# Performance work log

Hardware: AMD Instinct MI355X
Metric: run time of the kernel (lower is better)

## Reference

```python
import jax, jax.numpy as jnp
import numpy as np

N_NODES = 50000
N_EDGES = 800000
IN_CH = 256
OUT_CH = 64  # heads=1
NEG_SLOPE = 0.2


def setup_inputs() -> dict:
    key = jax.random.key(0)
    k1, k2, k3, k4, k5 = jax.random.split(key, 5)
    x = jax.random.normal(k1, (N_NODES, IN_CH), dtype=jnp.float32)
    edge_index = jax.random.randint(k2, (2, N_EDGES), 0, N_NODES, dtype=jnp.int64)
    # glorot init for dense weight [out, in] (torch Linear layout) and att [out, 2]
    s_w = np.sqrt(6.0 / (OUT_CH + IN_CH)).astype(np.float32)
    W = jax.random.uniform(k3, (OUT_CH, IN_CH), minval=-s_w, maxval=s_w, dtype=jnp.float32)
    b = jnp.zeros((OUT_CH,), dtype=jnp.float32)
    s_a = np.sqrt(6.0 / (OUT_CH + 2)).astype(np.float32)
    att = jax.random.uniform(k4, (OUT_CH, 2), minval=-s_a, maxval=s_a, dtype=jnp.float32)
    return {"x": x, "edge_index": edge_index, "W": W, "b": b, "att": att}


def reference(x, edge_index, W, b, att):
    n = x.shape[0]
    # dense projection: feature [N, OUT_CH]
    feature = x @ W.T + b
    # per-node attention contributions: e_pre [N, 2]
    e_pre = feature @ att
    tar = edge_index[0]  # flow='target_to_source'
    src = edge_index[1]
    # edge logit = leakyrelu(a_tar(t) + a_src(s)); self-loop logit per node
    logit_edge = jax.nn.leaky_relu(e_pre[tar, 0] + e_pre[src, 1], NEG_SLOPE)
    logit_self = jax.nn.leaky_relu(e_pre[:, 0] + e_pre[:, 1], NEG_SLOPE)
    # segment softmax over {self edge} U {incoming edges} per target node
    m = jnp.maximum(jax.ops.segment_max(logit_edge, tar, num_segments=n), logit_self)
    exp_edge = jnp.exp(logit_edge - m[tar])
    exp_self = jnp.exp(logit_self - m)
    denom = exp_self + jax.ops.segment_sum(exp_edge, tar, num_segments=n)
    alpha = exp_edge / denom[tar]          # [E]
    alpha_self = exp_self / denom          # [N]
    # weighted gather-scatter aggregation (fused_gas_agg)
    msgs = alpha[:, None] * feature[src]   # [E, OUT_CH]
    out = alpha_self[:, None] * feature + jax.ops.segment_sum(msgs, tar, num_segments=n)
    return out
```

## Files before the change

### kernel.cpp

```cpp
#include <hip/hip_runtime.h>
#include <math.h>

#define N_NODES 50000
#define N_EDGES 800000
#define IN_CH 256
#define OUT_CH 64
#define NEG_SLOPE 0.2f
#define PAD 64
#define DEGS 16

#define EDGE_BLOCKS 196
#define GEMM_BLOCKS 782

typedef __bf16 bf16x4 __attribute__((ext_vector_type(4)));
typedef __bf16 bf16x8 __attribute__((ext_vector_type(8)));
typedef float  f32x4  __attribute__((ext_vector_type(4)));

__global__ __launch_bounds__(256) void k_zero(int* __restrict__ deg)
{
    int idx = (blockIdx.x * 256 + threadIdx.x) * 4;
    if (idx + 4 <= N_NODES * DEGS)
        *reinterpret_cast<int4*>(&deg[idx]) = make_int4(0, 0, 0, 0);
}

__global__ __launch_bounds__(256) void k_fused(
    const float* __restrict__ x, const float* __restrict__ W,
    const float* __restrict__ bias, const float* __restrict__ att,
    const int* __restrict__ ei,
    __bf16* __restrict__ featb, float* __restrict__ e0,
    float* __restrict__ e1, int* __restrict__ deg,
    unsigned short* __restrict__ pcsr)
{
    __shared__ __bf16 B[64][264];

    const int t = threadIdx.x;

    if (blockIdx.x < EDGE_BLOCKS) {
        const int base = blockIdx.x * 4096 + t * 4;
        int tn[16], sn[16], sl[16];
        #pragma unroll
        for (int c = 0; c < 4; ++c) {
            int e = base + c * 1024;
            if (e + 4 <= N_EDGES) {
                *reinterpret_cast<int4*>(&tn[c * 4]) =
                    *reinterpret_cast<const int4*>(&ei[e]);
                *reinterpret_cast<int4*>(&sn[c * 4]) =
                    *reinterpret_cast<const int4*>(&ei[N_EDGES + e]);
            } else {
                #pragma unroll
                for (int j = 0; j < 4; ++j) {
                    int ee = e + j;
                    tn[c * 4 + j] = (ee < N_EDGES) ? ei[ee] : -1;
                    sn[c * 4 + j] = (ee < N_EDGES) ? ei[N_EDGES + ee] : 0;
                }
            }
        }
        #pragma unroll
        for (int k = 0; k < 16; ++k)
            sl[k] = (tn[k] >= 0) ? atomicAdd(&deg[tn[k] * DEGS], 1) : 0x7fffffff;
        #pragma unroll
        for (int k = 0; k < 16; ++k)
            if (tn[k] >= 0 && sl[k] < PAD)
                pcsr[(size_t)tn[k] * PAD + sl[k]] = (unsigned short)sn[k];
        return;
    }

    const int row0 = (blockIdx.x - EDGE_BLOCKS) * 64;
    const int wv   = t >> 6;
    const int li   = t & 63;
    const int lm   = li & 15;
    const int lq   = li >> 4;

    {
        const int sr = t >> 2;
        const int cq = t & 3;
        #pragma unroll
        for (int j = 0; j < 4; ++j) {
            #pragma unroll
            for (int i = 0; i < 4; ++i) {
                int kk = j * 64 + cq * 16 + i * 4;
                float4 w1 = *reinterpret_cast<const float4*>(&W[(size_t)sr * IN_CH + kk]);
                bf16x4 g = {(__bf16)w1.x, (__bf16)w1.y, (__bf16)w1.z, (__bf16)w1.w};
                *reinterpret_cast<bf16x4*>(&B[sr][kk]) = g;
            }
        }
    }
    __syncthreads();

    const int myrow = row0 + wv * 16 + lm;
    const float* xrow = x + (size_t)(myrow < N_NODES ? myrow : 0) * IN_CH;

    f32x4 acc[4];
    #pragma unroll
    for (int tn = 0; tn < 4; ++tn) acc[tn] = (f32x4){0.f, 0.f, 0.f, 0.f};

    #pragma unroll
    for (int kb = 0; kb < 8; ++kb) {
        int ko = kb * 32 + lq * 8;
        float4 a0 = *reinterpret_cast<const float4*>(&xrow[ko]);
        float4 a1 = *reinterpret_cast<const float4*>(&xrow[ko + 4]);
        bf16x8 a = {(__bf16)a0.x, (__bf16)a0.y, (__bf16)a0.z, (__bf16)a0.w,
                    (__bf16)a1.x, (__bf16)a1.y, (__bf16)a1.z, (__bf16)a1.w};
        #pragma unroll
        for (int tn = 0; tn < 4; ++tn) {
            bf16x8 b = *reinterpret_cast<const bf16x8*>(&B[tn * 16 + lm][ko]);
            acc[tn] = __builtin_amdgcn_mfma_f32_16x16x32_bf16(a, b, acc[tn], 0, 0, 0);
        }
    }

    float att0[4], att1[4], bv[4];
    #pragma unroll
    for (int tn = 0; tn < 4; ++tn) {
        int c = tn * 16 + lm;
        att0[tn] = att[c * 2 + 0];
        att1[tn] = att[c * 2 + 1];
        bv[tn]   = bias[c];
    }

    float p0[4] = {0.f, 0.f, 0.f, 0.f};
    float p1[4] = {0.f, 0.f, 0.f, 0.f};
    #pragma unroll
    for (int r = 0; r < 4; ++r) {
        int row = row0 + wv * 16 + lq * 4 + r;
        #pragma unroll
        for (int tn = 0; tn < 4; ++tn) {
            float f = acc[tn][r] + bv[tn];
            if (row < N_NODES)
                featb[(size_t)row * OUT_CH + tn * 16 + lm] = (__bf16)f;
            p0[r] += f * att0[tn];
            p1[r] += f * att1[tn];
        }
    }

    #pragma unroll
    for (int m = 1; m < 16; m <<= 1) {
        #pragma unroll
        for (int r = 0; r < 4; ++r) {
            p0[r] += __shfl_xor(p0[r], m, 64);
            p1[r] += __shfl_xor(p1[r], m, 64);
        }
    }
    if (lm == 0) {
        #pragma unroll
        for (int r = 0; r < 4; ++r) {
            int row = row0 + wv * 16 + lq * 4 + r;
            if (row < N_NODES) {
                e0[row] = p0[r];
                e1[row] = p1[r];
            }
        }
    }
}

__global__ __launch_bounds__(256) void k_gather(
    const float* __restrict__ e0, const float* __restrict__ e1,
    const __bf16* __restrict__ featb, const int* __restrict__ deg,
    const unsigned short* __restrict__ pcsr, float* __restrict__ out)
{
    int t    = blockIdx.x * 4 + (threadIdx.x >> 6);
    int lane = threadIdx.x & 63;
    if (t >= N_NODES) return;

    const int g  = lane >> 4;
    const int cl = lane & 15;

    int cnt = deg[t * DEGS];
    cnt = cnt > PAD ? PAD : cnt;

    float e0t = e0[t];

    int si = (int)pcsr[(size_t)t * PAD + lane];
    si = (lane < cnt) ? si : 0;
    float qi = e1[si];
    float zi = e0t + qi;
    float wi = (lane < cnt) ? __expf(zi > 0.f ? zi : NEG_SLOPE * zi) : 0.f;

    float zs  = e0t + e1[t];
    float wsf = __expf(zs > 0.f ? zs : NEG_SLOPE * zs);
    bf16x4 sf = *reinterpret_cast<const bf16x4*>(&featb[(size_t)t * OUT_CH + cl * 4]);

    float wsum = wi;
    #pragma unroll
    for (int m = 1; m < 64; m <<= 1)
        wsum += __shfl_xor(wsum, m, 64);
    wsum += wsf;

    f32x4 acc = {0.f, 0.f, 0.f, 0.f};
    int i = 0;
    for (; i + 16 <= cnt; i += 16) {
        float a0 = 0.f, a1 = 0.f, a2 = 0.f, a3 = 0.f;
        int   s0 = __shfl(si, i + g,      64);
        int   s1 = __shfl(si, i + 4 + g,  64);
        int   s2 = __shfl(si, i + 8 + g,  64);
        int   s3 = __shfl(si, i + 12 + g, 64);
        float w0 = __shfl(wi, i + g,      64);
        float w1 = __shfl(wi, i + 4 + g,  64);
        float w2 = __shfl(wi, i + 8 + g,  64);
        float w3 = __shfl(wi, i + 12 + g, 64);
        bf16x4 f0 = *reinterpret_cast<const bf16x4*>(&featb[(size_t)s0 * OUT_CH + cl * 4]);
        bf16x4 f1 = *reinterpret_cast<const bf16x4*>(&featb[(size_t)s1 * OUT_CH + cl * 4]);
        bf16x4 f2 = *reinterpret_cast<const bf16x4*>(&featb[(size_t)s2 * OUT_CH + cl * 4]);
        bf16x4 f3 = *reinterpret_cast<const bf16x4*>(&featb[(size_t)s3 * OUT_CH + cl * 4]);
        #pragma unroll
        for (int j = 0; j < 4; ++j) {
            a0 += 0.f;
            acc[j] += w0 * (float)f0[j] + w1 * (float)f1[j]
                    + w2 * (float)f2[j] + w3 * (float)f3[j];
        }
        (void)a0; (void)a1; (void)a2; (void)a3;
    }
    #pragma unroll 2
    for (; i < cnt; i += 4) {
        int   s0 = __shfl(si, i + g, 64);
        float w0 = __shfl(wi, i + g, 64);
        bf16x4 f0 = *reinterpret_cast<const bf16x4*>(&featb[(size_t)s0 * OUT_CH + cl * 4]);
        #pragma unroll
        for (int j = 0; j < 4; ++j)
            acc[j] += w0 * (float)f0[j];
    }

    #pragma unroll
    for (int j = 0; j < 4; ++j) {
        acc[j] += __shfl_xor(acc[j], 16, 64);
        acc[j] += __shfl_xor(acc[j], 32, 64);
    }

    if (g == 0) {
        float inv = 1.f / wsum;
        float4 o;
        o.x = (acc[0] + wsf * (float)sf[0]) * inv;
        o.y = (acc[1] + wsf * (float)sf[1]) * inv;
        o.z = (acc[2] + wsf * (float)sf[2]) * inv;
        o.w = (acc[3] + wsf * (float)sf[3]) * inv;
        *reinterpret_cast<float4*>(&out[(size_t)t * OUT_CH + cl * 4]) = o;
    }
}

extern "C" void kernel_launch(void* const* d_in, const int* in_sizes, int n_in,
                              void* d_out, int out_size, void* d_ws, size_t ws_size,
                              hipStream_t stream)
{
    const float* x    = (const float*)d_in[0];
    const int*   ei   = (const int*)d_in[1];
    const float* W    = (const float*)d_in[2];
    const float* bias = (const float*)d_in[3];
    const float* att  = (const float*)d_in[4];
    float* out = (float*)d_out;

    __bf16* featb = (__bf16*)d_ws;
    float*  e0    = (float*)(featb + (size_t)N_NODES * OUT_CH);
    float*  e1    = e0 + N_NODES;
    int*    deg   = (int*)(e1 + N_NODES);
    unsigned short* pcsr = (unsigned short*)(deg + (size_t)N_NODES * DEGS);

    dim3 blk(256);

    k_zero<<<dim3((N_NODES * DEGS / 4 + 255) / 256), blk, 0, stream>>>(deg);

    k_fused<<<dim3(EDGE_BLOCKS + GEMM_BLOCKS), blk, 0, stream>>>(
        x, W, bias, att, ei, featb, e0, e1, deg, pcsr);

    k_gather<<<dim3((N_NODES + 3) / 4), blk, 0, stream>>>(
        e0, e1, featb, deg, pcsr, out);
}
```

Baseline: 162.6 us.

## Stage e1 as fp16 in LDS and make gather a persistent grid-stride kernel

Result: slower. 175.3 us (+7.8%).

```diff
diff --git a/kernel.cpp b/kernel.cpp
--- a/kernel.cpp
+++ b/kernel.cpp
@@ -12,9 +12,13 @@
 #define EDGE_BLOCKS 196
 #define GEMM_BLOCKS 782
 
+#define GATHER_BLOCKS 256
+#define GATHER_THREADS 1024
+
 typedef __bf16 bf16x4 __attribute__((ext_vector_type(4)));
 typedef __bf16 bf16x8 __attribute__((ext_vector_type(8)));
 typedef float  f32x4  __attribute__((ext_vector_type(4)));
+typedef _Float16 f16x4 __attribute__((ext_vector_type(4)));
 
 __global__ __launch_bounds__(256) void k_zero(int* __restrict__ deg)
 {
@@ -152,87 +156,96 @@
     }
 }
 
-__global__ __launch_bounds__(256) void k_gather(
+__global__ __launch_bounds__(GATHER_THREADS) void k_gather(
     const float* __restrict__ e0, const float* __restrict__ e1,
     const __bf16* __restrict__ featb, const int* __restrict__ deg,
     const unsigned short* __restrict__ pcsr, float* __restrict__ out)
 {
-    int t    = blockIdx.x * 4 + (threadIdx.x >> 6);
-    int lane = threadIdx.x & 63;
-    if (t >= N_NODES) return;
-
-    const int g  = lane >> 4;
-    const int cl = lane & 15;
-
-    int cnt = deg[t * DEGS];
-    cnt = cnt > PAD ? PAD : cnt;
-
-    float e0t = e0[t];
-
-    int si = (int)pcsr[(size_t)t * PAD + lane];
-    si = (lane < cnt) ? si : 0;
-    float qi = e1[si];
-    float zi = e0t + qi;
-    float wi = (lane < cnt) ? __expf(zi > 0.f ? zi : NEG_SLOPE * zi) : 0.f;
-
-    float zs  = e0t + e1[t];
-    float wsf = __expf(zs > 0.f ? zs : NEG_SLOPE * zs);
-    bf16x4 sf = *reinterpret_cast<const bf16x4*>(&featb[(size_t)t * OUT_CH + cl * 4]);
-
-    float wsum = wi;
-    #pragma unroll
-    for (int m = 1; m < 64; m <<= 1)
-        wsum += __shfl_xor(wsum, m, 64);
-    wsum += wsf;
-
-    f32x4 acc = {0.f, 0.f, 0.f, 0.f};
-    int i = 0;
-    for (; i + 16 <= cnt; i += 16) {
-        float a0 = 0.f, a1 = 0.f, a2 = 0.f, a3 = 0.f;
-        int   s0 = __shfl(si, i + g,      64);
-        int   s1 = __shfl(si, i + 4 + g,  64);
-        int   s2 = __shfl(si, i + 8 + g,  64);
-        int   s3 = __shfl(si, i + 12 + g, 64);
-        float w0 = __shfl(wi, i + g,      64);
-        float w1 = __shfl(wi, i + 4 + g,  64);
-        float w2 = __shfl(wi, i + 8 + g,  64);
-        float w3 = __shfl(wi, i + 12 + g, 64);
-        bf16x4 f0 = *reinterpret_cast<const bf16x4*>(&featb[(size_t)s0 * OUT_CH + cl * 4]);
-        bf16x4 f1 = *reinterpret_cast<const bf16x4*>(&featb[(size_t)s1 * OUT_CH + cl * 4]);
-        bf16x4 f2 = *reinterpret_cast<const bf16x4*>(&featb[(size_t)s2 * OUT_CH + cl * 4]);
-        bf16x4 f3 = *reinterpret_cast<const bf16x4*>(&featb[(size_t)s3 * OUT_CH + cl * 4]);
+    __shared__ _Float16 e1h[N_NODES];
+
+    const int tid = threadIdx.x;
+
+    for (int i = tid; i < N_NODES / 4; i += GATHER_THREADS) {
+        float4 v = *reinterpret_cast<const float4*>(&e1[i * 4]);
+        f16x4 h = {(_Float16)v.x, (_Float16)v.y, (_Float16)v.z, (_Float16)v.w};
+        *reinterpret_cast<f16x4*>(&e1h[i * 4]) = h;
+    }
+    __syncthreads();
+
+    const int lane = tid & 63;
+    const int g    = lane >> 4;
+    const int cl   = lane & 15;
+    const int wstride = GATHER_BLOCKS * (GATHER_THREADS / 64);
+
+    for (int t = blockIdx.x * (GATHER_THREADS / 64) + (tid >> 6);
+         t < N_NODES; t += wstride) {
+
+        int cnt = deg[t * DEGS];
+        cnt = cnt > PAD ? PAD : cnt;
+
+        float e0t = e0[t];
+
+        int si = (int)pcsr[(size_t)t * PAD + lane];
+        si = (lane < cnt) ? si : 0;
+        float qi = (float)e1h[si];
+        float zi = e0t + qi;
+        float wi = (lane < cnt) ? __expf(zi > 0.f ? zi : NEG_SLOPE * zi) : 0.f;
+
+        float zs  = e0t + (float)e1h[t];
+        float wsf = __expf(zs > 0.f ? zs : NEG_SLOPE * zs);
+        bf16x4 sf = *reinterpret_cast<const bf16x4*>(&featb[(size_t)t * OUT_CH + cl * 4]);
+
+        float wsum = wi;
+        #pragma unroll
+        for (int m = 1; m < 64; m <<= 1)
+            wsum += __shfl_xor(wsum, m, 64);
+        wsum += wsf;
+
+        f32x4 acc = {0.f, 0.f, 0.f, 0.f};
+        int i = 0;
+        for (; i + 16 <= cnt; i += 16) {
+            int   s0 = __shfl(si, i + g,      64);
+            int   s1 = __shfl(si, i + 4 + g,  64);
+            int   s2 = __shfl(si, i + 8 + g,  64);
+            int   s3 = __shfl(si, i + 12 + g, 64);
+            float w0 = __shfl(wi, i + g,      64);
+            float w1 = __shfl(wi, i + 4 + g,  64);
+            float w2 = __shfl(wi, i + 8 + g,  64);
+            float w3 = __shfl(wi, i + 12 + g, 64);
+            bf16x4 f0 = *reinterpret_cast<const bf16x4*>(&featb[(size_t)s0 * OUT_CH + cl * 4]);
+            bf16x4 f1 = *reinterpret_cast<const bf16x4*>(&featb[(size_t)s1 * OUT_CH + cl * 4]);
+            bf16x4 f2 = *reinterpret_cast<const bf16x4*>(&featb[(size_t)s2 * OUT_CH + cl * 4]);
+            bf16x4 f3 = *reinterpret_cast<const bf16x4*>(&featb[(size_t)s3 * OUT_CH + cl * 4]);
+            #pragma unroll
+            for (int j = 0; j < 4; ++j)
+                acc[j] += w0 * (float)f0[j] + w1 * (float)f1[j]
+                        + w2 * (float)f2[j] + w3 * (float)f3[j];
+        }
+        #pragma unroll 2
+        for (; i < cnt; i += 4) {
+            int   s0 = __shfl(si, i + g, 64);
+            float w0 = __shfl(wi, i + g, 64);
+            bf16x4 f0 = *reinterpret_cast<const bf16x4*>(&featb[(size_t)s0 * OUT_CH + cl * 4]);
+            #pragma unroll
+            for (int j = 0; j < 4; ++j)
+                acc[j] += w0 * (float)f0[j];
+        }
+
         #pragma unroll
         for (int j = 0; j < 4; ++j) {
-            a0 += 0.f;
-            acc[j] += w0 * (float)f0[j] + w1 * (float)f1[j]
-                    + w2 * (float)f2[j] + w3 * (float)f3[j];
-        }
-        (void)a0; (void)a1; (void)a2; (void)a3;
-    }
-    #pragma unroll 2
-    for (; i < cnt; i += 4) {
-        int   s0 = __shfl(si, i + g, 64);
-        float w0 = __shfl(wi, i + g, 64);
-        bf16x4 f0 = *reinterpret_cast<const bf16x4*>(&featb[(size_t)s0 * OUT_CH + cl * 4]);
-        #pragma unroll
-        for (int j = 0; j < 4; ++j)
-            acc[j] += w0 * (float)f0[j];
-    }
-
-    #pragma unroll
-    for (int j = 0; j < 4; ++j) {
-        acc[j] += __shfl_xor(acc[j], 16, 64);
-        acc[j] += __shfl_xor(acc[j], 32, 64);
-    }
-
-    if (g == 0) {
-        float inv = 1.f / wsum;
-        float4 o;
-        o.x = (acc[0] + wsf * (float)sf[0]) * inv;
-        o.y = (acc[1] + wsf * (float)sf[1]) * inv;
-        o.z = (acc[2] + wsf * (float)sf[2]) * inv;
-        o.w = (acc[3] + wsf * (float)sf[3]) * inv;
-        *reinterpret_cast<float4*>(&out[(size_t)t * OUT_CH + cl * 4]) = o;
+            acc[j] += __shfl_xor(acc[j], 16, 64);
+            acc[j] += __shfl_xor(acc[j], 32, 64);
+        }
+
+        if (g == 0) {
+            float inv = 1.f / wsum;
+            float4 o;
+            o.x = (acc[0] + wsf * (float)sf[0]) * inv;
+            o.y = (acc[1] + wsf * (float)sf[1]) * inv;
+            o.z = (acc[2] + wsf * (float)sf[2]) * inv;
+            o.w = (acc[3] + wsf * (float)sf[3]) * inv;
+            *reinterpret_cast<float4*>(&out[(size_t)t * OUT_CH + cl * 4]) = o;
+        }
     }
 }
 
@@ -260,6 +273,6 @@
     k_fused<<<dim3(EDGE_BLOCKS + GEMM_BLOCKS), blk, 0, stream>>>(
         x, W, bias, att, ei, featb, e0, e1, deg, pcsr);
 
-    k_gather<<<dim3((N_NODES + 3) / 4), blk, 0, stream>>>(
+    k_gather<<<dim3(GATHER_BLOCKS), dim3(GATHER_THREADS), 0, stream>>>(
         e0, e1, featb, deg, pcsr, out);
 }
```
